# Performance work log

Hardware: AMD Instinct MI355X
Metric: run time of the kernel (lower is better)

Reference implementation:

```python
import jax, jax.numpy as jnp
import numpy as np

GROUPS = 32
EPS = 1e-5


def setup_inputs() -> dict:
    key = jax.random.key(0)
    k1, k2, k3, k4, k5 = jax.random.split(key, 5)
    B, C, H, W = 16, 256, 80, 80
    cg = C // GROUPS  # 8 channels per group
    x = jax.random.normal(k1, (B, C, H, W), dtype=jnp.float32)
    # conv1x1: Conv2d(cg, cg, 1) -> weight [cg, cg], bias [cg]
    fan_in = cg
    bound = 1.0 / np.sqrt(fan_in)
    conv_w = jax.random.uniform(k2, (cg, cg), minval=-bound, maxval=bound, dtype=jnp.float32)
    conv_b = jax.random.uniform(k3, (cg,), minval=-bound, maxval=bound, dtype=jnp.float32)
    # GroupNorm(num_groups=cg, num_channels=cg) affine params (init: ones/zeros)
    gn_w = jnp.ones((cg,), dtype=jnp.float32)
    gn_b = jnp.zeros((cg,), dtype=jnp.float32)
    return {"x": x, "conv_w": conv_w, "conv_b": conv_b, "gn_w": gn_w, "gn_b": gn_b}


def reference(x, conv_w, conv_b, gn_w, gn_b):
    b, c, h, w = x.shape
    cg = c // GROUPS
    gx = x.reshape(b * GROUPS, cg, h, w)  # [bg, cg, h, w]

    def norm(t):
        # GroupNorm with num_groups == num_channels: per-channel norm over (h, w)
        mu = jnp.mean(t, axis=(2, 3), keepdims=True)
        var = jnp.var(t, axis=(2, 3), keepdims=True)
        tn = (t - mu) * jax.lax.rsqrt(var + EPS)
        return tn * gn_w[None, :, None, None] + gn_b[None, :, None, None]

    def gate_branch(ph, pw):
        # ph: [bg, cg, h] (pooled over w), pw: [bg, cg, w] (pooled over h)
        cat = jnp.concatenate([ph, pw], axis=2)  # [bg, cg, h+w]
        hw = jnp.einsum('bcl,oc->bol', cat, conv_w) + conv_b[None, :, None]
        gh, gw = hw[:, :, :h], hw[:, :, h:]
        gated = gx * jax.nn.sigmoid(gh)[..., None] * jax.nn.sigmoid(gw)[:, :, None, :]
        return norm(gated)

    # avg-pool branch
    x1 = gate_branch(jnp.mean(gx, axis=3), jnp.mean(gx, axis=2))
    # max-pool branch
    y1 = gate_branch(jnp.max(gx, axis=3), jnp.max(gx, axis=2))

    x11 = x1.reshape(b * GROUPS, cg, h * w)
    y11 = y1.reshape(b * GROUPS, cg, h * w)
    # channel-attention vectors: softmax over the cg channel axis
    x12 = jax.nn.softmax(jnp.mean(x1, axis=(2, 3)), axis=-1)  # [bg, cg]  (avg pool)
    y12 = jax.nn.softmax(jnp.max(y1, axis=(2, 3)), axis=-1)   # [bg, cg]  (max pool)

    weights = jnp.einsum('bc,bcl->bl', x12, y11) + jnp.einsum('bc,bcl->bl', y12, x11)
    weights = weights.reshape(b * GROUPS, 1, h, w)
    return (gx * jax.nn.sigmoid(weights)).reshape(b, c, h, w)
```

## Files before the change

kernel.cpp:

```cpp
#include <hip/hip_runtime.h>
#include <math.h>

constexpr int CG   = 8;
constexpr int Hh   = 80;
constexpr int HW   = 6400;
constexpr int NG   = 512;
constexpr int NCH  = NG * CG;
constexpr int PP   = NCH * 80;
constexpr float EPSf = 1e-5f;

__device__ __forceinline__ float sigmoidf(float v) {
    return 1.0f / (1.0f + __expf(-v));
}

__global__ __launch_bounds__(256) void k_pool(const float* __restrict__ x,
                                              float* __restrict__ ws) {
    const int bgc = blockIdx.x;
    const float* base = x + (size_t)bgc * HW;
    __shared__ float tile[Hh * 84];

    for (int v = threadIdx.x; v < 1600; v += 256) {
        int h  = v / 20;
        int w0 = (v % 20) * 4;
        float4 d = ((const float4*)base)[v];
        *(float4*)&tile[h * 84 + w0] = d;
    }
    __syncthreads();

    const int t = threadIdx.x;
    if (t < 80) {
        float s = 0.f, m = -INFINITY;
        const float4* r = (const float4*)&tile[t * 84];
        #pragma unroll
        for (int i = 0; i < 20; i++) {
            float4 d = r[i];
            s += d.x + d.y + d.z + d.w;
            m = fmaxf(m, fmaxf(fmaxf(d.x, d.y), fmaxf(d.z, d.w)));
        }
        ws[0 * PP + bgc * 80 + t] = s * (1.f / 80.f);
        ws[2 * PP + bgc * 80 + t] = m;
    } else if (t >= 128 && t < 208) {
        const int c = t - 128;
        float s2 = 0.f, m2 = -INFINITY;
        #pragma unroll 8
        for (int i = 0; i < 80; i++) {
            float v = tile[i * 84 + c];
            s2 += v;
            m2 = fmaxf(m2, v);
        }
        ws[1 * PP + bgc * 80 + c] = s2 * (1.f / 80.f);
        ws[3 * PP + bgc * 80 + c] = m2;
    }
}

__global__ __launch_bounds__(1024, 4) void k_rest(
    const float* __restrict__ x,
    const float* __restrict__ conv_w,
    const float* __restrict__ conv_b,
    const float* __restrict__ gnw,
    const float* __restrict__ gnb,
    const float* __restrict__ ws,
    float* __restrict__ out)
{
    const int bg  = blockIdx.x;
    const int tid = threadIdx.x;

    __shared__ float pl[2560];
    __shared__ float g[2560];
    __shared__ float wsm[64];
    __shared__ float cbs[8];
    __shared__ float red[16][6];
    __shared__ float Axs[8], Bxs[8], Ays[8], Bys[8], ymaxs[8], cHx[8], cHy[8];
    __shared__ float kcs;

    if (tid < 64) wsm[tid] = conv_w[tid];
    if (tid < 8)  cbs[tid] = conv_b[tid];
    #pragma unroll
    for (int i = 0; i < 3; ++i) {
        const int e = tid + i * 1024;
        if (e < 2560) {
            const int a = e / 640, rem = e % 640, c = rem / 80, p = rem % 80;
            pl[e] = ws[a * PP + (bg * 8 + c) * 80 + p];
        }
    }
    __syncthreads();

    #pragma unroll
    for (int i = 0; i < 3; ++i) {
        const int e = tid + i * 1024;
        if (e < 2560) {
            const int a = e / 640, rem = e % 640, c = rem / 80, p = rem % 80;
            float acc = cbs[c];
            #pragma unroll
            for (int cc = 0; cc < 8; ++cc)
                acc += wsm[c * 8 + cc] * pl[a * 640 + cc * 80 + p];
            g[e] = sigmoidf(acc);
        }
    }
    __syncthreads();

    const float* base = x + (size_t)bg * CG * HW;
    {
        const int c = tid >> 7, sl = tid & 127;
        const float* cb_ = base + c * HW;
        float s1x = 0.f, s2x = 0.f, s1y = 0.f, s2y = 0.f;
        float my = -INFINITY, ny = INFINITY;
        #pragma unroll 4
        for (int j = 0; j < 13; ++j) {
            const int v = sl + j * 128;
            if (v < 1600) {
                float4 d = ((const float4*)cb_)[v];
                const int h = v / 20, w0 = (v % 20) * 4;
                const float ghx = g[0 * 640 + c * 80 + h];
                const float ghy = g[2 * 640 + c * 80 + h];
                const float4 gwx = *(const float4*)&g[1 * 640 + c * 80 + w0];
                const float4 gwy = *(const float4*)&g[3 * 640 + c * 80 + w0];
                const float dd[4]  = {d.x, d.y, d.z, d.w};
                const float gx4[4] = {gwx.x, gwx.y, gwx.z, gwx.w};
                const float gy4[4] = {gwy.x, gwy.y, gwy.z, gwy.w};
                #pragma unroll
                for (int k = 0; k < 4; ++k) {
                    const float tx = dd[k] * ghx * gx4[k];
                    const float ty = dd[k] * ghy * gy4[k];
                    s1x += tx; s2x += tx * tx;
                    s1y += ty; s2y += ty * ty;
                    my = fmaxf(my, ty); ny = fminf(ny, ty);
                }
            }
        }
        #pragma unroll
        for (int off = 32; off > 0; off >>= 1) {
            s1x += __shfl_down(s1x, off);
            s2x += __shfl_down(s2x, off);
            s1y += __shfl_down(s1y, off);
            s2y += __shfl_down(s2y, off);
            my = fmaxf(my, __shfl_down(my, off));
            ny = fminf(ny, __shfl_down(ny, off));
        }
        const int wv = tid >> 6;
        if ((tid & 63) == 0) {
            red[wv][0] = s1x; red[wv][1] = s2x; red[wv][2] = s1y;
            red[wv][3] = s2y; red[wv][4] = my;  red[wv][5] = ny;
        }
    }
    __syncthreads();

    if (tid < 8) {
        const float s1x = red[2 * tid][0] + red[2 * tid + 1][0];
        const float s2x = red[2 * tid][1] + red[2 * tid + 1][1];
        const float s1y = red[2 * tid][2] + red[2 * tid + 1][2];
        const float s2y = red[2 * tid][3] + red[2 * tid + 1][3];
        const float my  = fmaxf(red[2 * tid][4], red[2 * tid + 1][4]);
        const float ny  = fminf(red[2 * tid][5], red[2 * tid + 1][5]);
        const float w = gnw[tid], b = gnb[tid];
        const float mux  = s1x * (1.f / 6400.f);
        const float varx = s2x * (1.f / 6400.f) - mux * mux;
        const float ax   = rsqrtf(varx + EPSf) * w;
        Axs[tid] = ax; Bxs[tid] = b - mux * ax;
        const float muy  = s1y * (1.f / 6400.f);
        const float vary = s2y * (1.f / 6400.f) - muy * muy;
        const float ay   = rsqrtf(vary + EPSf) * w;
        Ays[tid] = ay; Bys[tid] = b - muy * ay;
        ymaxs[tid] = (ay >= 0.f ? my : ny) * ay + Bys[tid];
    }
    __syncthreads();
    if (tid == 0) {
        float x12[8], y12[8];
        float mb = -INFINITY;
        for (int c = 0; c < 8; ++c) mb = fmaxf(mb, gnb[c]);
        float se = 0.f;
        for (int c = 0; c < 8; ++c) { x12[c] = __expf(gnb[c] - mb); se += x12[c]; }
        float inv = 1.f / se;
        for (int c = 0; c < 8; ++c) x12[c] *= inv;
        float m2 = -INFINITY;
        for (int c = 0; c < 8; ++c) m2 = fmaxf(m2, ymaxs[c]);
        se = 0.f;
        for (int c = 0; c < 8; ++c) { y12[c] = __expf(ymaxs[c] - m2); se += y12[c]; }
        inv = 1.f / se;
        float kc = 0.f;
        for (int c = 0; c < 8; ++c) {
            y12[c] *= inv;
            cHx[c] = y12[c] * Axs[c];
            cHy[c] = x12[c] * Ays[c];
            kc += x12[c] * Bys[c] + y12[c] * Bxs[c];
        }
        kcs = kc;
    }
    __syncthreads();
    if (tid < 640) {
        g[tid]        *= cHx[tid / 80];
        g[1280 + tid] *= cHy[tid / 80];
    }
    __syncthreads();

    const float kc = kcs;
    float* ob = out + (size_t)bg * CG * HW;
    #pragma unroll
    for (int i = 0; i < 2; ++i) {
        const int v = tid + i * 1024;
        if (v < 1600) {
            const int h = v / 20, w0 = (v % 20) * 4;
            float4 gxv[8];
            #pragma unroll
            for (int c = 0; c < 8; ++c)
                gxv[c] = ((const float4*)(base + c * HW))[v];

            float s0 = kc, s1 = kc, s2 = kc, s3 = kc;
            #pragma unroll
            for (int c = 0; c < 8; ++c) {
                const float chx = g[c * 80 + h];
                const float chy = g[1280 + c * 80 + h];
                const float4 cwx = *(const float4*)&g[640  + c * 80 + w0];
                const float4 cwy = *(const float4*)&g[1920 + c * 80 + w0];
                s0 += gxv[c].x * (chy * cwy.x + chx * cwx.x);
                s1 += gxv[c].y * (chy * cwy.y + chx * cwx.y);
                s2 += gxv[c].z * (chy * cwy.z + chx * cwx.z);
                s3 += gxv[c].w * (chy * cwy.w + chx * cwx.w);
            }
            s0 = sigmoidf(s0); s1 = sigmoidf(s1);
            s2 = sigmoidf(s2); s3 = sigmoidf(s3);
            #pragma unroll
            for (int c = 0; c < 8; ++c) {
                float4 o;
                o.x = gxv[c].x * s0; o.y = gxv[c].y * s1;
                o.z = gxv[c].z * s2; o.w = gxv[c].w * s3;
                ((float4*)(ob + c * HW))[v] = o;
            }
        }
    }
}

extern "C" void kernel_launch(void* const* d_in, const int* in_sizes, int n_in,
                              void* d_out, int out_size, void* d_ws, size_t ws_size,
                              hipStream_t stream) {
    const float* x      = (const float*)d_in[0];
    const float* conv_w = (const float*)d_in[1];
    const float* conv_b = (const float*)d_in[2];
    const float* gn_w   = (const float*)d_in[3];
    const float* gn_b   = (const float*)d_in[4];
    float* out = (float*)d_out;
    float* ws  = (float*)d_ws;

    k_pool<<<NCH, 256, 0, stream>>>(x, ws);
    k_rest<<<NG, 1024, 0, stream>>>(x, conv_w, conv_b, gn_w, gn_b, ws, out);
}
```

Measured before the change: 72.58 us.

## Split each group across two 512-thread blocks that redundantly compute stats

k_rest now launches two 512-thread blocks per group instead of one 1024-thread block. Each block recomputes the pooled conv gates and the full GroupNorm statistics over the whole group, then writes only its half of the output pixels. The aim is more, smaller blocks for better occupancy and load balance across CUs. The cost is that the statistics pass, which reads the full 8x6400 input of the group, runs twice, increasing global reads.

```diff
diff --git a/kernel.cpp b/kernel.cpp
--- a/kernel.cpp
+++ b/kernel.cpp
@@ -53,7 +53,7 @@
     }
 }
 
-__global__ __launch_bounds__(1024, 4) void k_rest(
+__global__ __launch_bounds__(512, 8) void k_rest(
     const float* __restrict__ x,
     const float* __restrict__ conv_w,
     const float* __restrict__ conv_b,
@@ -62,22 +62,23 @@
     const float* __restrict__ ws,
     float* __restrict__ out)
 {
-    const int bg  = blockIdx.x;
-    const int tid = threadIdx.x;
+    const int bg   = blockIdx.x >> 1;
+    const int half = blockIdx.x & 1;
+    const int tid  = threadIdx.x;
 
     __shared__ float pl[2560];
     __shared__ float g[2560];
     __shared__ float wsm[64];
     __shared__ float cbs[8];
-    __shared__ float red[16][6];
+    __shared__ float red[8][6];
     __shared__ float Axs[8], Bxs[8], Ays[8], Bys[8], ymaxs[8], cHx[8], cHy[8];
     __shared__ float kcs;
 
     if (tid < 64) wsm[tid] = conv_w[tid];
     if (tid < 8)  cbs[tid] = conv_b[tid];
     #pragma unroll
-    for (int i = 0; i < 3; ++i) {
-        const int e = tid + i * 1024;
+    for (int i = 0; i < 5; ++i) {
+        const int e = tid + i * 512;
         if (e < 2560) {
             const int a = e / 640, rem = e % 640, c = rem / 80, p = rem % 80;
             pl[e] = ws[a * PP + (bg * 8 + c) * 80 + p];
@@ -86,8 +87,8 @@
     __syncthreads();
 
     #pragma unroll
-    for (int i = 0; i < 3; ++i) {
-        const int e = tid + i * 1024;
+    for (int i = 0; i < 5; ++i) {
+        const int e = tid + i * 512;
         if (e < 2560) {
             const int a = e / 640, rem = e % 640, c = rem / 80, p = rem % 80;
             float acc = cbs[c];
@@ -101,31 +102,28 @@
 
     const float* base = x + (size_t)bg * CG * HW;
     {
-        const int c = tid >> 7, sl = tid & 127;
+        const int c = tid >> 6, lane = tid & 63;
         const float* cb_ = base + c * HW;
         float s1x = 0.f, s2x = 0.f, s1y = 0.f, s2y = 0.f;
         float my = -INFINITY, ny = INFINITY;
-        #pragma unroll 4
-        for (int j = 0; j < 13; ++j) {
-            const int v = sl + j * 128;
-            if (v < 1600) {
-                float4 d = ((const float4*)cb_)[v];
-                const int h = v / 20, w0 = (v % 20) * 4;
-                const float ghx = g[0 * 640 + c * 80 + h];
-                const float ghy = g[2 * 640 + c * 80 + h];
-                const float4 gwx = *(const float4*)&g[1 * 640 + c * 80 + w0];
-                const float4 gwy = *(const float4*)&g[3 * 640 + c * 80 + w0];
-                const float dd[4]  = {d.x, d.y, d.z, d.w};
-                const float gx4[4] = {gwx.x, gwx.y, gwx.z, gwx.w};
-                const float gy4[4] = {gwy.x, gwy.y, gwy.z, gwy.w};
-                #pragma unroll
-                for (int k = 0; k < 4; ++k) {
-                    const float tx = dd[k] * ghx * gx4[k];
-                    const float ty = dd[k] * ghy * gy4[k];
-                    s1x += tx; s2x += tx * tx;
-                    s1y += ty; s2y += ty * ty;
-                    my = fmaxf(my, ty); ny = fminf(ny, ty);
-                }
+        for (int j = 0; j < 25; ++j) {
+            const int v = lane + j * 64;
+            float4 d = ((const float4*)cb_)[v];
+            const int h = v / 20, w0 = (v % 20) * 4;
+            const float ghx = g[0 * 640 + c * 80 + h];
+            const float ghy = g[2 * 640 + c * 80 + h];
+            const float4 gwx = *(const float4*)&g[1 * 640 + c * 80 + w0];
+            const float4 gwy = *(const float4*)&g[3 * 640 + c * 80 + w0];
+            const float dd[4]  = {d.x, d.y, d.z, d.w};
+            const float gx4[4] = {gwx.x, gwx.y, gwx.z, gwx.w};
+            const float gy4[4] = {gwy.x, gwy.y, gwy.z, gwy.w};
+            #pragma unroll
+            for (int k = 0; k < 4; ++k) {
+                const float tx = dd[k] * ghx * gx4[k];
+                const float ty = dd[k] * ghy * gy4[k];
+                s1x += tx; s2x += tx * tx;
+                s1y += ty; s2y += ty * ty;
+                my = fmaxf(my, ty); ny = fminf(ny, ty);
             }
         }
         #pragma unroll
@@ -137,21 +135,17 @@
             my = fmaxf(my, __shfl_down(my, off));
             ny = fminf(ny, __shfl_down(ny, off));
         }
-        const int wv = tid >> 6;
-        if ((tid & 63) == 0) {
-            red[wv][0] = s1x; red[wv][1] = s2x; red[wv][2] = s1y;
-            red[wv][3] = s2y; red[wv][4] = my;  red[wv][5] = ny;
+        if (lane == 0) {
+            red[c][0] = s1x; red[c][1] = s2x; red[c][2] = s1y;
+            red[c][3] = s2y; red[c][4] = my;  red[c][5] = ny;
         }
     }
     __syncthreads();
 
     if (tid < 8) {
-        const float s1x = red[2 * tid][0] + red[2 * tid + 1][0];
-        const float s2x = red[2 * tid][1] + red[2 * tid + 1][1];
-        const float s1y = red[2 * tid][2] + red[2 * tid + 1][2];
-        const float s2y = red[2 * tid][3] + red[2 * tid + 1][3];
-        const float my  = fmaxf(red[2 * tid][4], red[2 * tid + 1][4]);
-        const float ny  = fminf(red[2 * tid][5], red[2 * tid + 1][5]);
+        const float s1x = red[tid][0], s2x = red[tid][1];
+        const float s1y = red[tid][2], s2y = red[tid][3];
+        const float my  = red[tid][4], ny  = red[tid][5];
         const float w = gnw[tid], b = gnb[tid];
         const float mux  = s1x * (1.f / 6400.f);
         const float varx = s2x * (1.f / 6400.f) - mux * mux;
@@ -187,9 +181,9 @@
         kcs = kc;
     }
     __syncthreads();
-    if (tid < 640) {
-        g[tid]        *= cHx[tid / 80];
-        g[1280 + tid] *= cHy[tid / 80];
+    for (int e = tid; e < 640; e += 512) {
+        g[e]        *= cHx[e / 80];
+        g[1280 + e] *= cHy[e / 80];
     }
     __syncthreads();
 
@@ -197,8 +191,9 @@
     float* ob = out + (size_t)bg * CG * HW;
     #pragma unroll
     for (int i = 0; i < 2; ++i) {
-        const int v = tid + i * 1024;
-        if (v < 1600) {
+        const int r = tid + i * 512;
+        if (r < 800) {
+            const int v = half * 800 + r;
             const int h = v / 20, w0 = (v % 20) * 4;
             float4 gxv[8];
             #pragma unroll
@@ -241,6 +236,6 @@
     float* out = (float*)d_out;
     float* ws  = (float*)d_ws;
 
-    k_pool<<<NCH, 256, 0, stream>>>(x, ws);
-    k_rest<<<NG, 1024, 0, stream>>>(x, conv_w, conv_b, gn_w, gn_b, ws, out);
-}
+    k_pool<<<NCH,    256, 0, stream>>>(x, ws);
+    k_rest<<<NG * 2, 512, 0, stream>>>(x, conv_w, conv_b, gn_w, gn_b, ws, out);
+}
```

New measurement: 103.4 us. 1.43x slower.
